# Performance work log

Measured on AMD Instinct MI355X. Metric: run time of the kernel, lower is better.

The kernel has to match this reference:

```python
import jax, jax.numpy as jnp
import numpy as np
import math

L = 6        # num_layers
H = 16       # nhead
D = 1024     # feature_dim (= d_model, dim_factor=1)
DFF = 1024
IN = 1024    # input_dim
B, T = 16, 512
HD = D // H
EPS = 1e-5


def _get_slopes(n):
    def pow2(n):
        start = 2.0 ** (-2.0 ** (-(math.log2(n) - 3)))
        return [start * (start ** i) for i in range(n)]
    if math.log2(n).is_integer():
        return pow2(n)
    cp2 = 2 ** math.floor(math.log2(n))
    return pow2(cp2) + _get_slopes(2 * cp2)[0::2][: n - cp2]


def _alibi_bias(num_heads, seq_len):
    # init_alibi_biased_mask_future reduces to -slope_h * |i - j|
    slopes = jnp.asarray(_get_slopes(num_heads), dtype=jnp.float32)  # [H]
    idx = jnp.arange(seq_len)
    rel = -jnp.abs(idx[:, None] - idx[None, :]).astype(jnp.float32)  # [T,T]
    return slopes[:, None, None] * rel  # [H,T,T]


def _ln(x, w, b):
    m = jnp.mean(x, axis=-1, keepdims=True)
    v = jnp.mean(jnp.square(x - m), axis=-1, keepdims=True)
    return (x - m) * jax.lax.rsqrt(v + EPS) * w + b


def setup_inputs() -> dict:
    key = jax.random.key(0)
    ks = jax.random.split(key, 16)
    s = 0.02
    return {
        "x": jax.random.normal(ks[0], (B, T, IN), dtype=jnp.float32),
        "bn_w": jax.random.normal(ks[1], (D, IN), dtype=jnp.float32) * s,
        "bn_b": jnp.zeros((D,), jnp.float32),
        "qkv_w": jax.random.normal(ks[2], (L, 3 * D, D), dtype=jnp.float32) * s,
        "qkv_b": jnp.zeros((L, 3 * D), jnp.float32),
        "out_w": jax.random.normal(ks[3], (L, D, D), dtype=jnp.float32) * s,
        "out_b": jnp.zeros((L, D), jnp.float32),
        "ln1_w": jnp.ones((L, D), jnp.float32),
        "ln1_b": jnp.zeros((L, D), jnp.float32),
        "ln2_w": jnp.ones((L, D), jnp.float32),
        "ln2_b": jnp.zeros((L, D), jnp.float32),
        "ff1_w": jax.random.normal(ks[4], (L, DFF, D), dtype=jnp.float32) * s,
        "ff1_b": jnp.zeros((L, DFF), jnp.float32),
        "ff2_w": jax.random.normal(ks[5], (L, D, DFF), dtype=jnp.float32) * s,
        "ff2_b": jnp.zeros((L, D), jnp.float32),
    }


def reference(x, bn_w, bn_b, qkv_w, qkv_b, out_w, out_b,
              ln1_w, ln1_b, ln2_w, ln2_b, ff1_w, ff1_b, ff2_w, ff2_b):
    b, t, _ = x.shape
    bias = _alibi_bias(H, t)  # [H,T,T], same for all batch elements
    h = x @ bn_w.T + bn_b  # bottleneck -> [B,T,D]
    scale = 1.0 / math.sqrt(HD)
    for l in range(L):
        qkv = h @ qkv_w[l].T + qkv_b[l]  # [B,T,3D]
        q, k, v = jnp.split(qkv, 3, axis=-1)
        q = q.reshape(b, t, H, HD)
        k = k.reshape(b, t, H, HD)
        v = v.reshape(b, t, H, HD)
        scores = jnp.einsum('bihd,bjhd->bhij', q, k) * scale + bias[None]
        attn = jax.nn.softmax(scores, axis=-1)
        o = jnp.einsum('bhij,bjhd->bihd', attn, v).reshape(b, t, D)
        o = o @ out_w[l].T + out_b[l]
        h = _ln(h + o, ln1_w[l], ln1_b[l])  # post-norm (PyTorch default)
        f = jax.nn.gelu(h @ ff1_w[l].T + ff1_b[l], approximate=False)
        f = f @ ff2_w[l].T + ff2_b[l]
        h = _ln(h + f, ln2_w[l], ln2_b[l])
    return h
```

## Files before the change

### kernel.cpp

```cpp
#include <hip/hip_runtime.h>
#include <stdint.h>

#define DEV static __device__ __forceinline__

typedef __attribute__((ext_vector_type(8))) uint16_t u16x8;
typedef __attribute__((ext_vector_type(4))) uint16_t u16x4;
typedef __attribute__((ext_vector_type(4))) uint32_t u32x4;
typedef __attribute__((ext_vector_type(4))) float    f32x4;
typedef __attribute__((ext_vector_type(8))) __bf16   bf16x8;

typedef __attribute__((address_space(3))) void lds_void;
typedef __attribute__((address_space(1))) void gbl_void;

DEV float bf2f(uint16_t u){
  union { uint32_t i; float f; } v; v.i = ((uint32_t)u) << 16; return v.f;
}
DEV uint16_t f2bf(float f){ return __builtin_bit_cast(uint16_t, (__bf16)f); }
DEV f32x4 mfma16(u16x8 a, u16x8 b, f32x4 c){
  return __builtin_amdgcn_mfma_f32_16x16x32_bf16(
      __builtin_bit_cast(bf16x8, a), __builtin_bit_cast(bf16x8, b), c, 0, 0, 0);
}
DEV uint32_t cvt_pk_bf16(float lo, float hi){
  uint32_t r;
  asm("v_cvt_pk_bf16_f32 %0, %1, %2" : "=v"(r) : "v"(lo), "v"(hi));
  return r;
}

__global__ __launch_bounds__(256)
void te_cvt(const float* __restrict__ in, uint16_t* __restrict__ out)
{
  const size_t i = ((size_t)blockIdx.x * 256 + threadIdx.x) * 8;
  f32x4 a = *(const f32x4*)(in + i);
  f32x4 b = *(const f32x4*)(in + i + 4);
  u16x8 o;
#pragma unroll
  for (int e = 0; e < 4; e++) {
    o[e]     = f2bf(a[e]);
    o[e + 4] = f2bf(b[e]);
  }
  *(u16x8*)(out + i) = o;
}

template<int MODE>
__global__ __launch_bounds__(512)
void te_gemm256(const uint16_t* __restrict__ A, int lda,
                const uint16_t* __restrict__ Wm, const float* __restrict__ bias,
                uint16_t* __restrict__ outB, int N, int K)
{
  constexpr int SZA = 256 * 64;
  constexpr int SZB = 128 * 64;
  __shared__ uint16_t lds[2 * (SZA + SZB)];

  const int tid = threadIdx.x;
  const int w = tid >> 6, l = tid & 63;
  const int lr = l & 15, lg = l >> 4;
  const int wr = w >> 2, wc = w & 3;
  const int srow = l >> 3, chunk = l & 7;

  const int nb = gridDim.x;
  const int bid = blockIdx.x;
  const int lid = (bid & 7) * (nb >> 3) + (bid >> 3);
  const int nx = N >> 7;
  const int tm = (lid / nx) << 8;
  const int tn = (lid % nx) << 7;

  const int rw = w * 8 + srow;
  const int sc = (chunk ^ srow) << 3;

  auto stage = [&](int kt, int p) {
    const int k0 = kt << 6;
    uint16_t* bufA = lds + p * (SZA + SZB);
    uint16_t* bufB = bufA + SZA;
#pragma unroll
    for (int c = 0; c < 4; c++) {
      const uint16_t* ga = A + (size_t)(tm + c * 64 + rw) * lda + (k0 + sc);
      __builtin_amdgcn_global_load_lds((gbl_void*)(uintptr_t)ga,
          (lds_void*)(bufA + (c * 64 + w * 8) * 64), 16, 0, 0);
    }
#pragma unroll
    for (int c = 0; c < 2; c++) {
      const uint16_t* gw = Wm + (size_t)(tn + c * 64 + rw) * K + (k0 + sc);
      __builtin_amdgcn_global_load_lds((gbl_void*)(uintptr_t)gw,
          (lds_void*)(bufB + (c * 64 + w * 8) * 64), 16, 0, 0);
    }
  };

  f32x4 acc[8][2] = {};
  const int nt = K >> 6;

  stage(0, 0);
  for (int t = 0; t < nt; ++t) {
    const int cur = t & 1;
    uint16_t* bufA = lds + cur * (SZA + SZB);
    uint16_t* bufB = bufA + SZA;

    asm volatile("" ::: "memory");
    if (t + 1 < nt) {
      stage(t + 1, cur ^ 1);
      asm volatile("s_waitcnt vmcnt(6)" ::: "memory");
    } else {
      asm volatile("s_waitcnt vmcnt(0)" ::: "memory");
    }
    __builtin_amdgcn_s_barrier();

    u16x8 bf[2][2];
#pragma unroll
    for (int fc = 0; fc < 2; fc++)
#pragma unroll
      for (int kk = 0; kk < 2; kk++) {
        const int nrow = wc * 32 + fc * 16 + lr;
        bf[fc][kk] = *(const u16x8*)&bufB[nrow * 64 + (((kk * 4 + lg) ^ (lr & 7)) << 3)];
      }

#pragma unroll
    for (int q = 0; q < 4; q++) {
      u16x8 af[2][2];
#pragma unroll
      for (int i = 0; i < 2; i++)
#pragma unroll
        for (int kk = 0; kk < 2; kk++) {
          const int row = wr * 128 + (q * 2 + i) * 16 + lr;
          af[i][kk] = *(const u16x8*)&bufA[row * 64 + (((kk * 4 + lg) ^ (lr & 7)) << 3)];
        }
      __builtin_amdgcn_s_barrier();
      __builtin_amdgcn_s_setprio(1);
#pragma unroll
      for (int i = 0; i < 2; i++)
#pragma unroll
        for (int fc = 0; fc < 2; fc++) {
          acc[q * 2 + i][fc] = mfma16(af[i][0], bf[fc][0], acc[q * 2 + i][fc]);
          acc[q * 2 + i][fc] = mfma16(af[i][1], bf[fc][1], acc[q * 2 + i][fc]);
        }
      __builtin_amdgcn_s_setprio(0);
      __builtin_amdgcn_s_barrier();
    }
  }

  float bv[2];
#pragma unroll
  for (int fc = 0; fc < 2; fc++) bv[fc] = bias[tn + wc * 32 + fc * 16 + lr];
#pragma unroll
  for (int fr = 0; fr < 8; fr++)
#pragma unroll
    for (int fc = 0; fc < 2; fc++)
#pragma unroll
      for (int r = 0; r < 4; r++) {
        const int row = tm + wr * 128 + fr * 16 + lg * 4 + r;
        const int col = tn + wc * 32 + fc * 16 + lr;
        float v = acc[fr][fc][r] + bv[fc];
        if (MODE == 2) {
          const float u = 0.7978845608028654f * v * (1.0f + 0.044715f * v * v);
          const float t = 1.0f - 2.0f / (__expf(2.0f * u) + 1.0f);
          v = 0.5f * v * (1.0f + t);
        }
        outB[(size_t)row * N + col] = f2bf(v);
      }
}

#define SOFTMAX_PACK(S, MR, SDQ, ACC, IQ, P2)                                  \
  {                                                                            \
    const float f0 = (float)((IQ) - jt - lg * 4);                              \
    float mt = -1e30f;                                                         \
    _Pragma("unroll")                                                          \
    for (int n = 0; n < 4; n++) {                                              \
      const float fj = f0 - (float)(n * 16);                                   \
      _Pragma("unroll")                                                        \
      for (int r = 0; r < 4; r++) {                                            \
        const float v = fmaf(S[n][r], scl2e, -slope2e * fabsf(fj - (float)r)); \
        S[n][r] = v;                                                           \
        mt = fmaxf(mt, v);                                                     \
      }                                                                        \
    }                                                                          \
    mt = fmaxf(mt, __shfl_xor(mt, 16));                                        \
    mt = fmaxf(mt, __shfl_xor(mt, 32));                                        \
    if (!__all(mt <= MR)) {                                                    \
      const float mN = fmaxf(MR, mt);                                          \
      const float fq = exp2f(MR - mN);                                         \
      MR = mN;                                                                 \
      SDQ *= fq;                                                               \
      float fA[4];                                                             \
      _Pragma("unroll")                                                        \
      for (int r = 0; r < 4; r++) fA[r] = __shfl(fq, lg * 4 + r);              \
      _Pragma("unroll")                                                        \
      for (int n = 0; n < 4; n++)                                              \
        _Pragma("unroll")                                                      \
        for (int r = 0; r < 4; r++) ACC[n][r] *= fA[r];                        \
    }                                                                          \
    float rs = 0.0f;                                                           \
    _Pragma("unroll")                                                          \
    for (int n = 0; n < 4; n++)                                                \
      _Pragma("unroll")                                                        \
      for (int r = 0; r < 4; r++) {                                            \
        const float p = exp2f(S[n][r] - MR);                                   \
        S[n][r] = p;                                                           \
        rs += p;                                                               \
      }                                                                        \
    rs += __shfl_xor(rs, 16);                                                  \
    rs += __shfl_xor(rs, 32);                                                  \
    SDQ += rs;                                                                 \
    _Pragma("unroll")                                                          \
    for (int n = 0; n < 4; n++) {                                              \
      P2[n][0] = cvt_pk_bf16(S[n][0], S[n][1]);                                \
      P2[n][1] = cvt_pk_bf16(S[n][2], S[n][3]);                                \
    }                                                                          \
  }

__global__ __launch_bounds__(256)
void te_attn(uint16_t* __restrict__ qkv)
{
  __shared__ uint16_t kl[64 * 64];
  __shared__ uint16_t vt[64 * 64];
  const int tid = threadIdx.x;
  const int w = tid >> 6, l = tid & 63;
  const int lr = l & 15, lg = l >> 4;
  const int bh = blockIdx.x, qt = blockIdx.y;
  const int h = bh & 15, b = bh >> 4;

  const int iQ0 = qt * 128 + w * 16 + lr;
  u16x8 qf[2][2];
#pragma unroll
  for (int g = 0; g < 2; g++) {
    const size_t qoff = ((size_t)(b * 512 + iQ0 + g * 64)) * 3072 + h * 64 + lg * 8;
    qf[g][0] = *(const u16x8*)&qkv[qoff];
    qf[g][1] = *(const u16x8*)&qkv[qoff + 32];
  }
  const float LOG2E = 1.4426950408889634f;
  const float scl2e = 0.125f * LOG2E;
  const float slope2e = exp2f(-0.5f * (float)(h + 1)) * LOG2E;

  const int sjb = tid >> 3;
  const int sd0 = (tid & 7) * 8;

  float mR0 = -1e30f, sdq0 = 0.0f, mR1 = -1e30f, sdq1 = 0.0f;
  f32x4 acc0[4] = {}, acc1[4] = {};

  u16x8 kreg[2], vreg[2];
  {
    const int jt0 = (qt * 2) * 64;
#pragma unroll
    for (int cc = 0; cc < 2; cc++) {
      const int j = sjb + cc * 32;
      const size_t rbase = ((size_t)(b * 512 + jt0 + j)) * 3072 + h * 64 + sd0;
      kreg[cc] = *(const u16x8*)&qkv[rbase + 1024];
      vreg[cc] = *(const u16x8*)&qkv[rbase + 2048];
    }
  }

  for (int step = 0; step < 8; step++) {
    const int jt = ((qt * 2 + step) & 7) * 64;
#pragma unroll
    for (int cc = 0; cc < 2; cc++) {
      const int j = sjb + cc * 32;
      *(u16x8*)&kl[j * 64 + (((sd0 >> 3) ^ (j & 7)) << 3)] = kreg[cc];
      const int cV = (((j >> 3) ^ (sd0 >> 3)) << 3) + (j & 7);
#pragma unroll
      for (int e = 0; e < 8; e++) vt[(sd0 + e) * 64 + cV] = vreg[cc][e];
    }
    __syncthreads();
    if (step < 7) {
      const int jtn = ((qt * 2 + step + 1) & 7) * 64;
#pragma unroll
      for (int cc = 0; cc < 2; cc++) {
        const int j = sjb + cc * 32;
        const size_t rbase = ((size_t)(b * 512 + jtn + j)) * 3072 + h * 64 + sd0;
        kreg[cc] = *(const u16x8*)&qkv[rbase + 1024];
        vreg[cc] = *(const u16x8*)&qkv[rbase + 2048];
      }
    }

    f32x4 s0[4] = {}, s1[4] = {};
#pragma unroll
    for (int kk = 0; kk < 2; kk++) {
      u16x8 kf[4];
#pragma unroll
      for (int n = 0; n < 4; n++) {
        const int row = n * 16 + lr;
        kf[n] = *(const u16x8*)&kl[row * 64 + (((kk * 4 + lg) ^ (lr & 7)) << 3)];
      }
      __builtin_amdgcn_s_setprio(1);
#pragma unroll
      for (int n = 0; n < 4; n++) {
        s0[n] = mfma16(kf[n], qf[0][kk], s0[n]);
        s1[n] = mfma16(kf[n], qf[1][kk], s1[n]);
      }
      __builtin_amdgcn_s_setprio(0);
    }

    uint32_t P2a[4][2], P2b[4][2];
    SOFTMAX_PACK(s0, mR0, sdq0, acc0, iQ0,      P2a);
    SOFTMAX_PACK(s1, mR1, sdq1, acc1, iQ0 + 64, P2b);

#pragma unroll
    for (int kk = 0; kk < 2; kk++) {
      uint32_t pw0[4], pw1[4];
#pragma unroll
      for (int t = 0; t < 4; t++) {
        const int srcLane = lr + 16 * ((lg & 1) * 2 + (t >> 1));
        const uint32_t a0 = __shfl(P2a[2 * kk + 0][t & 1], srcLane);
        const uint32_t b0 = __shfl(P2a[2 * kk + 1][t & 1], srcLane);
        pw0[t] = (lg >> 1) ? b0 : a0;
        const uint32_t a1 = __shfl(P2b[2 * kk + 0][t & 1], srcLane);
        const uint32_t b1 = __shfl(P2b[2 * kk + 1][t & 1], srcLane);
        pw1[t] = (lg >> 1) ? b1 : a1;
      }
      u32x4 q0 = { pw0[0], pw0[1], pw0[2], pw0[3] };
      u32x4 q1 = { pw1[0], pw1[1], pw1[2], pw1[3] };
      u16x8 pf0 = __builtin_bit_cast(u16x8, q0);
      u16x8 pf1 = __builtin_bit_cast(u16x8, q1);
      u16x8 vf[4];
#pragma unroll
      for (int n = 0; n < 4; n++) {
        const int row = n * 16 + lr;
        vf[n] = *(const u16x8*)&vt[row * 64 + ((((kk * 4 + lg) ^ (2 * n + (lr >> 3))) & 7) << 3)];
      }
      __builtin_amdgcn_s_setprio(1);
#pragma unroll
      for (int n = 0; n < 4; n++) {
        acc0[n] = mfma16(pf0, vf[n], acc0[n]);
        acc1[n] = mfma16(pf1, vf[n], acc1[n]);
      }
      __builtin_amdgcn_s_setprio(0);
    }
    __syncthreads();
  }

  {
    float sdA[4];
#pragma unroll
    for (int r = 0; r < 4; r++) sdA[r] = 1.0f / __shfl(sdq0, lg * 4 + r);
#pragma unroll
    for (int n = 0; n < 4; n++)
#pragma unroll
      for (int r = 0; r < 4; r++) {
        const int i = qt * 128 + w * 16 + lg * 4 + r;
        const int d = h * 64 + n * 16 + lr;
        qkv[((size_t)(b * 512 + i)) * 3072 + d] = f2bf(acc0[n][r] * sdA[r]);
      }
  }
  {
    float sdA[4];
#pragma unroll
    for (int r = 0; r < 4; r++) sdA[r] = 1.0f / __shfl(sdq1, lg * 4 + r);
#pragma unroll
    for (int n = 0; n < 4; n++)
#pragma unroll
      for (int r = 0; r < 4; r++) {
        const int i = qt * 128 + 64 + w * 16 + lg * 4 + r;
        const int d = h * 64 + n * 16 + lr;
        qkv[((size_t)(b * 512 + i)) * 3072 + d] = f2bf(acc1[n][r] * sdA[r]);
      }
  }
}

template<int FINAL>
__global__ __launch_bounds__(256)
void te_ln(const uint16_t* __restrict__ h, const uint16_t* __restrict__ delta,
           const float* __restrict__ w, const float* __restrict__ b,
           uint16_t* __restrict__ hout, float* __restrict__ fout)
{
  const int row = blockIdx.x, t = threadIdx.x;
  const size_t base = (size_t)row * 1024 + t * 4;
  u16x4 hv = *(const u16x4*)&h[base];
  u16x4 dv = *(const u16x4*)&delta[base];
  float x[4];
#pragma unroll
  for (int i = 0; i < 4; i++) x[i] = bf2f(hv[i]) + bf2f(dv[i]);
  float s = x[0] + x[1] + x[2] + x[3];
  float ss = x[0]*x[0] + x[1]*x[1] + x[2]*x[2] + x[3]*x[3];
#pragma unroll
  for (int msk = 32; msk >= 1; msk >>= 1) {
    s  += __shfl_xor(s, msk);
    ss += __shfl_xor(ss, msk);
  }
  __shared__ float rs[4], rq[4];
  const int wv = t >> 6;
  if ((t & 63) == 0) { rs[wv] = s; rq[wv] = ss; }
  __syncthreads();
  s  = rs[0] + rs[1] + rs[2] + rs[3];
  ss = rq[0] + rq[1] + rq[2] + rq[3];
  const float mean = s * (1.0f / 1024.0f);
  const float var  = ss * (1.0f / 1024.0f) - mean * mean;
  const float rstd = rsqrtf(var + 1e-5f);
  f32x4 wv4 = *(const f32x4*)&w[t * 4];
  f32x4 bv4 = *(const f32x4*)&b[t * 4];
  if (FINAL == 0) {
    u16x4 bo;
#pragma unroll
    for (int i = 0; i < 4; i++)
      bo[i] = f2bf((x[i] - mean) * rstd * wv4[i] + bv4[i]);
    *(u16x4*)&hout[base] = bo;
  } else {
    f32x4 yo;
#pragma unroll
    for (int i = 0; i < 4; i++)
      yo[i] = (x[i] - mean) * rstd * wv4[i] + bv4[i];
    *(f32x4*)&fout[base] = yo;
  }
}

extern "C" void kernel_launch(void* const* d_in, const int* in_sizes, int n_in,
                              void* d_out, int out_size, void* d_ws, size_t ws_size,
                              hipStream_t stream)
{
  (void)in_sizes; (void)n_in; (void)out_size; (void)ws_size;
  const float* x     = (const float*)d_in[0];
  const float* bn_w  = (const float*)d_in[1];
  const float* bn_b  = (const float*)d_in[2];
  const float* qkv_w = (const float*)d_in[3];
  const float* qkv_b = (const float*)d_in[4];
  const float* out_w = (const float*)d_in[5];
  const float* out_b = (const float*)d_in[6];
  const float* ln1_w = (const float*)d_in[7];
  const float* ln1_b = (const float*)d_in[8];
  const float* ln2_w = (const float*)d_in[9];
  const float* ln2_b = (const float*)d_in[10];
  const float* ff1_w = (const float*)d_in[11];
  const float* ff1_b = (const float*)d_in[12];
  const float* ff2_w = (const float*)d_in[13];
  const float* ff2_b = (const float*)d_in[14];

  char* ws = (char*)d_ws;
  uint16_t* h_bf    = (uint16_t*)ws;
  uint16_t* qkvb    = (uint16_t*)(ws + (16u  << 20));
  uint16_t* scrA    = (uint16_t*)(ws + (64u  << 20));
  uint16_t* qkvw_bf = (uint16_t*)(ws + (80u  << 20));
  uint16_t* ff2w_bf = (uint16_t*)(ws + (116u << 20));
  uint16_t* bnw_bf  = (uint16_t*)(ws + (128u << 20));
  uint16_t* outw_bf = (uint16_t*)d_out;
  uint16_t* ff1w_bf = (uint16_t*)((char*)d_out + (12u << 20));
  float*    outf    = (float*)d_out;

  dim3 blk(256);
  dim3 blk512(512);

  te_cvt<<<dim3(18874368 / 2048), blk, 0, stream>>>(qkv_w, qkvw_bf);
  te_cvt<<<dim3(6291456  / 2048), blk, 0, stream>>>(out_w, outw_bf);
  te_cvt<<<dim3(6291456  / 2048), blk, 0, stream>>>(ff1_w, ff1w_bf);
  te_cvt<<<dim3(6291456  / 2048), blk, 0, stream>>>(ff2_w, ff2w_bf);
  te_cvt<<<dim3(1048576  / 2048), blk, 0, stream>>>(bn_w,  bnw_bf);
  te_cvt<<<dim3(8388608  / 2048), blk, 0, stream>>>(x,     scrA);

  te_gemm256<0><<<dim3(256), blk512, 0, stream>>>(scrA, 1024, bnw_bf, bn_b,
                                                  h_bf, 1024, 1024);

  for (int l = 0; l < 6; l++) {
    te_gemm256<0><<<dim3(768), blk512, 0, stream>>>(
        h_bf, 1024, qkvw_bf + (size_t)l * 3072 * 1024, qkv_b + l * 3072,
        qkvb, 3072, 1024);
    te_attn<<<dim3(256, 4), blk, 0, stream>>>(qkvb);
    te_gemm256<0><<<dim3(256), blk512, 0, stream>>>(
        qkvb, 3072, outw_bf + (size_t)l * 1024 * 1024, out_b + l * 1024,
        scrA, 1024, 1024);
    te_ln<0><<<dim3(8192), blk, 0, stream>>>(h_bf, scrA, ln1_w + l * 1024, ln1_b + l * 1024,
                                             h_bf, nullptr);
    te_gemm256<2><<<dim3(256), blk512, 0, stream>>>(
        h_bf, 1024, ff1w_bf + (size_t)l * 1024 * 1024, ff1_b + l * 1024,
        scrA, 1024, 1024);
    te_gemm256<0><<<dim3(256), blk512, 0, stream>>>(
        scrA, 1024, ff2w_bf + (size_t)l * 1024 * 1024, ff2_b + l * 1024,
        qkvb, 1024, 1024);
    if (l == 5) {
      te_ln<1><<<dim3(8192), blk, 0, stream>>>(h_bf, qkvb, ln2_w + l * 1024, ln2_b + l * 1024,
                                               nullptr, outf);
    } else {
      te_ln<0><<<dim3(8192), blk, 0, stream>>>(h_bf, qkvb, ln2_w + l * 1024, ln2_b + l * 1024,
                                               h_bf, nullptr);
    }
  }
}
```

Baseline: 1.404 ms.

## Triple-buffer GEMM LDS and remap warps to a 4x2 grid of 64x64 tiles

```diff
diff --git a/kernel.cpp b/kernel.cpp
--- a/kernel.cpp
+++ b/kernel.cpp
@@ -49,12 +49,12 @@
 {
   constexpr int SZA = 256 * 64;
   constexpr int SZB = 128 * 64;
-  __shared__ uint16_t lds[2 * (SZA + SZB)];
+  __shared__ uint16_t lds[3 * (SZA + SZB)];
 
   const int tid = threadIdx.x;
   const int w = tid >> 6, l = tid & 63;
   const int lr = l & 15, lg = l >> 4;
-  const int wr = w >> 2, wc = w & 3;
+  const int wr = w >> 1, wc = w & 1;
   const int srow = l >> 3, chunk = l & 7;
 
   const int nb = gridDim.x;
@@ -85,69 +85,71 @@
     }
   };
 
-  f32x4 acc[8][2] = {};
+  f32x4 acc[4][4] = {};
   const int nt = K >> 6;
 
   stage(0, 0);
+  stage(1, 1);
   for (int t = 0; t < nt; ++t) {
-    const int cur = t & 1;
+    const int cur = t % 3;
     uint16_t* bufA = lds + cur * (SZA + SZB);
     uint16_t* bufB = bufA + SZA;
 
     asm volatile("" ::: "memory");
-    if (t + 1 < nt) {
-      stage(t + 1, cur ^ 1);
+    if (t + 2 < nt) {
+      stage(t + 2, (t + 2) % 3);
+      asm volatile("s_waitcnt vmcnt(12)" ::: "memory");
+    } else if (t + 1 < nt) {
       asm volatile("s_waitcnt vmcnt(6)" ::: "memory");
     } else {
       asm volatile("s_waitcnt vmcnt(0)" ::: "memory");
     }
     __builtin_amdgcn_s_barrier();
 
-    u16x8 bf[2][2];
-#pragma unroll
-    for (int fc = 0; fc < 2; fc++)
-#pragma unroll
-      for (int kk = 0; kk < 2; kk++) {
-        const int nrow = wc * 32 + fc * 16 + lr;
-        bf[fc][kk] = *(const u16x8*)&bufB[nrow * 64 + (((kk * 4 + lg) ^ (lr & 7)) << 3)];
-      }
-
-#pragma unroll
-    for (int q = 0; q < 4; q++) {
-      u16x8 af[2][2];
-#pragma unroll
-      for (int i = 0; i < 2; i++)
-#pragma unroll
-        for (int kk = 0; kk < 2; kk++) {
-          const int row = wr * 128 + (q * 2 + i) * 16 + lr;
-          af[i][kk] = *(const u16x8*)&bufA[row * 64 + (((kk * 4 + lg) ^ (lr & 7)) << 3)];
-        }
-      __builtin_amdgcn_s_barrier();
+#pragma unroll
+    for (int kk = 0; kk < 2; kk++) {
+      u16x8 af[4], bfr[2];
+#pragma unroll
+      for (int i = 0; i < 4; i++) {
+        const int row = wr * 64 + i * 16 + lr;
+        af[i] = *(const u16x8*)&bufA[row * 64 + (((kk * 4 + lg) ^ (lr & 7)) << 3)];
+      }
+#pragma unroll
+      for (int j = 0; j < 2; j++) {
+        const int row = wc * 64 + j * 16 + lr;
+        bfr[j] = *(const u16x8*)&bufB[row * 64 + (((kk * 4 + lg) ^ (lr & 7)) << 3)];
+      }
+      u16x8 bfr2[2];
+#pragma unroll
+      for (int j = 0; j < 2; j++) {
+        const int row = wc * 64 + (j + 2) * 16 + lr;
+        bfr2[j] = *(const u16x8*)&bufB[row * 64 + (((kk * 4 + lg) ^ (lr & 7)) << 3)];
+      }
       __builtin_amdgcn_s_setprio(1);
 #pragma unroll
-      for (int i = 0; i < 2; i++)
-#pragma unroll
-        for (int fc = 0; fc < 2; fc++) {
-          acc[q * 2 + i][fc] = mfma16(af[i][0], bf[fc][0], acc[q * 2 + i][fc]);
-          acc[q * 2 + i][fc] = mfma16(af[i][1], bf[fc][1], acc[q * 2 + i][fc]);
-        }
+      for (int i = 0; i < 4; i++) {
+        acc[i][0] = mfma16(af[i], bfr[0],  acc[i][0]);
+        acc[i][1] = mfma16(af[i], bfr[1],  acc[i][1]);
+        acc[i][2] = mfma16(af[i], bfr2[0], acc[i][2]);
+        acc[i][3] = mfma16(af[i], bfr2[1], acc[i][3]);
+      }
       __builtin_amdgcn_s_setprio(0);
-      __builtin_amdgcn_s_barrier();
-    }
-  }
-
-  float bv[2];
-#pragma unroll
-  for (int fc = 0; fc < 2; fc++) bv[fc] = bias[tn + wc * 32 + fc * 16 + lr];
-#pragma unroll
-  for (int fr = 0; fr < 8; fr++)
-#pragma unroll
-    for (int fc = 0; fc < 2; fc++)
+    }
+    __builtin_amdgcn_s_barrier();
+  }
+
+  float bv[4];
+#pragma unroll
+  for (int j = 0; j < 4; j++) bv[j] = bias[tn + wc * 64 + j * 16 + lr];
+#pragma unroll
+  for (int i = 0; i < 4; i++)
+#pragma unroll
+    for (int j = 0; j < 4; j++)
 #pragma unroll
       for (int r = 0; r < 4; r++) {
-        const int row = tm + wr * 128 + fr * 16 + lg * 4 + r;
-        const int col = tn + wc * 32 + fc * 16 + lr;
-        float v = acc[fr][fc][r] + bv[fc];
+        const int row = tm + wr * 64 + i * 16 + lg * 4 + r;
+        const int col = tn + wc * 64 + j * 16 + lr;
+        float v = acc[i][j][r] + bv[j];
         if (MODE == 2) {
           const float u = 0.7978845608028654f * v * (1.0f + 0.044715f * v * v);
           const float t = 1.0f - 2.0f / (__expf(2.0f * u) + 1.0f);
```

New measurement: 1.386 ms. About the same (-1.2%).
